# Kernel tuning notes

Measured on AMD Instinct MI355X. Metric: run time of the kernel, lower is better.

## Reference

```python
import jax, jax.numpy as jnp
import numpy as np

B, C, H, W = 32, 256, 8, 8
N = H * W                      # n_objects = 64
D_G_IN = 2 * C + 2             # pair concat + 2-dim relative position = 514
HG = 512                       # g hidden / output dim
HF = 512                       # f hidden dim
D_OUT = 256                    # f output dim


def _relative_grid_feat():
    # feat[p, q, 0] = oh(p) - oh(q); feat[p, q, 1] = ow(p) - ow(q); zero-centered globally
    idx = jnp.arange(N)
    oh, ow = idx // W, idx % W
    r0 = (oh[:, None] - oh[None, :]).astype(jnp.float32)
    r1 = (ow[:, None] - ow[None, :]).astype(jnp.float32)
    rel = jnp.stack([r0, r1], axis=-1)  # [N, N, 2]
    return rel - rel.mean()


def setup_inputs() -> dict:
    key = jax.random.key(0)
    ks = jax.random.split(key, 11)
    s = 0.02
    return {
        "x": jax.random.normal(ks[0], (B, C, H, W), dtype=jnp.float32),
        "g_W0": jax.random.normal(ks[1], (D_G_IN, HG), dtype=jnp.float32) * s,
        "g_b0": jnp.zeros((HG,), dtype=jnp.float32),
        "g_W1": jax.random.normal(ks[2], (HG, HG), dtype=jnp.float32) * s,
        "g_b1": jnp.zeros((HG,), dtype=jnp.float32),
        "g_W2": jax.random.normal(ks[3], (HG, HG), dtype=jnp.float32) * s,
        "g_b2": jnp.zeros((HG,), dtype=jnp.float32),
        "f_W0": jax.random.normal(ks[4], (HG, HF), dtype=jnp.float32) * s,
        "f_b0": jnp.zeros((HF,), dtype=jnp.float32),
        "f_W1": jax.random.normal(ks[5], (HF, D_OUT), dtype=jnp.float32) * s,
        "f_b1": jnp.zeros((D_OUT,), dtype=jnp.float32),
    }


def reference(x, g_W0, g_b0, g_W1, g_b1, g_W2, g_b2, f_W0, f_b0, f_W1, f_b1):
    relu = jax.nn.relu
    x_flat = x.reshape(B, C, N)                     # [B, C, N]
    xT = jnp.transpose(x_flat, (0, 2, 1))           # [B, N, C]
    # pair index k = p*N + q: xi takes object q (inner), xj takes object p (outer)
    xi = jnp.broadcast_to(xT[:, None, :, :], (B, N, N, C))
    xj = jnp.broadcast_to(xT[:, :, None, :], (B, N, N, C))
    rel = jnp.broadcast_to(_relative_grid_feat()[None], (B, N, N, 2))
    pair = jnp.concatenate([xi, xj, rel], axis=-1)  # [B, N, N, 2C+2]
    # g MLP (nonlinear=True -> activation on output too)
    h = relu(jnp.einsum('bpqd,dh->bpqh', pair, g_W0) + g_b0)
    h = relu(jnp.einsum('bpqh,hk->bpqk', h, g_W1) + g_b1)
    relations = relu(jnp.einsum('bpqh,hk->bpqk', h, g_W2) + g_b2)  # [B, N, N, HG]
    embedding = relations.sum(axis=(1, 2))          # sum over all pairs -> [B, HG]
    # f MLP (linear output)
    hf = relu(embedding @ f_W0 + f_b0)
    out = hf @ f_W1 + f_b1                          # [B, D_OUT]
    return out
```

## Files before the change

kernel.cpp:

```cpp
#include <hip/hip_runtime.h>


typedef short short8 __attribute__((ext_vector_type(8)));
typedef float f32x16 __attribute__((ext_vector_type(16)));

__device__ __forceinline__ unsigned short f2bf(float f) {
    unsigned u = __builtin_bit_cast(unsigned, f);
    u = (u + 0x7FFFu + ((u >> 16) & 1u)) >> 16;
    return (unsigned short)u;
}

__device__ __forceinline__ unsigned cvt_pk(float a, float b) {
    unsigned r;
    asm("v_cvt_pk_bf16_f32 %0, %1, %2" : "=v"(r) : "v"(a), "v"(b));
    return r;
}

__global__ __launch_bounds__(512) void uv_kernel(
    const float* __restrict__ x, const float* __restrict__ W0,
    const float* __restrict__ b0, float* __restrict__ Up, float* __restrict__ Vp)
{
    __shared__ float xs[256 * 8];
    const int blk = blockIdx.x;
    const int b = blk >> 3, n0 = (blk & 7) * 8;
    const int tid = threadIdx.x;

    for (int i = tid; i < 2048; i += 512) {
        int c = i >> 3, r = i & 7;
        xs[i] = x[((size_t)b * 256 + c) * 64 + n0 + r];
    }
    __syncthreads();

    const int h = tid;
    float ua[8], va[8];
#pragma unroll
    for (int r = 0; r < 8; ++r) { ua[r] = 0.f; va[r] = 0.f; }

    for (int c = 0; c < 256; ++c) {
        float wa = W0[(size_t)c * 512 + h];
        float wb = W0[(size_t)(256 + c) * 512 + h];
#pragma unroll
        for (int r = 0; r < 8; ++r) {
            float xv = xs[c * 8 + r];
            ua[r] += xv * wa;
            va[r] += xv * wb;
        }
    }
    const float w2a = W0[(size_t)512 * 512 + h];
    const float w2b = W0[(size_t)513 * 512 + h];
    const float bb = b0[h];
#pragma unroll
    for (int r = 0; r < 8; ++r) {
        int n = n0 + r;
        float fh = (float)(n >> 3), fw = (float)(n & 7);
        Up[((size_t)b * 64 + n) * 512 + h] = ua[r] - fh * w2a - fw * w2b;
        Vp[((size_t)b * 64 + n) * 512 + h] = va[r] + fh * w2a + fw * w2b + bb;
    }
}

__global__ __launch_bounds__(256) void wswz_kernel(
    const float* __restrict__ W1, const float* __restrict__ W2,
    unsigned short* __restrict__ W1s, unsigned short* __restrict__ W2s,
    float* __restrict__ emb)
{
    int gid = blockIdx.x * 256 + threadIdx.x;
    if (gid < 16384) emb[gid] = 0.f;
    int m = gid >> 15;
    int idx = gid & 32767;
    int col = idx & 511;
    int kg = idx >> 9;
    const float* W = m ? W2 : W1;
    unsigned short* O = m ? W2s : W1s;
    short8 v;
#pragma unroll
    for (int j = 0; j < 8; ++j)
        v[j] = (short)f2bf(W[(size_t)(kg * 8 + j) * 512 + col]);
    *(short8*)(O + (size_t)idx * 8) = v;
}

__global__ __launch_bounds__(512, 2) void main_kernel(
    const float* __restrict__ Up, const float* __restrict__ Vp,
    const unsigned short* __restrict__ W1s, const unsigned short* __restrict__ W2s,
    const float* __restrict__ b1, const float* __restrict__ b2,
    float* __restrict__ emb)
{
    extern __shared__ __align__(16) unsigned char lds[];
    unsigned char* T[2] = { lds, lds + 65536 };

    const int wg = ((blockIdx.x & 7) << 7) | (blockIdx.x >> 3);
    const int b = wg >> 5, pp = wg & 31;
    const int p0 = pp * 2, p1 = p0 + 1;

    const int tid = threadIdx.x;
    const int lane = tid & 63, wave = tid >> 6;
    const int l31 = lane & 31, lg = lane >> 5;
    const int swz = (l31 & 15) << 4;
    const int wcol = wave * 64;

    {
        const int cc = tid & 63;
        const int r0 = tid >> 6;
        const float* vA = Vp + ((size_t)(b * 64 + p0)) * 512 + cc * 8;
        const float* vB = Vp + ((size_t)(b * 64 + p1)) * 512 + cc * 8;
        float4 vA0 = *(const float4*)(vA),     vA1 = *(const float4*)(vA + 4);
        float4 vB0 = *(const float4*)(vB),     vB1 = *(const float4*)(vB + 4);
#pragma unroll
        for (int it = 0; it < 8; ++it) {
            int row = r0 + it * 8;
            const float* ub = Up + ((size_t)(b * 64 + row)) * 512 + cc * 8;
            float4 u0 = *(const float4*)(ub);
            float4 u1 = *(const float4*)(ub + 4);
            int off = row * 1024 + ((cc * 16) ^ ((row & 15) << 4));
            uint4 w;
            w.x = cvt_pk(fmaxf(u0.x + vA0.x, 0.f), fmaxf(u0.y + vA0.y, 0.f));
            w.y = cvt_pk(fmaxf(u0.z + vA0.z, 0.f), fmaxf(u0.w + vA0.w, 0.f));
            w.z = cvt_pk(fmaxf(u1.x + vA1.x, 0.f), fmaxf(u1.y + vA1.y, 0.f));
            w.w = cvt_pk(fmaxf(u1.z + vA1.z, 0.f), fmaxf(u1.w + vA1.w, 0.f));
            *(uint4*)(&T[0][off]) = w;
            w.x = cvt_pk(fmaxf(u0.x + vB0.x, 0.f), fmaxf(u0.y + vB0.y, 0.f));
            w.y = cvt_pk(fmaxf(u0.z + vB0.z, 0.f), fmaxf(u0.w + vB0.w, 0.f));
            w.z = cvt_pk(fmaxf(u1.x + vB1.x, 0.f), fmaxf(u1.y + vB1.y, 0.f));
            w.w = cvt_pk(fmaxf(u1.z + vB1.z, 0.f), fmaxf(u1.w + vB1.w, 0.f));
            *(uint4*)(&T[1][off]) = w;
        }
    }
    __syncthreads();

    const int arow0 = l31 * 1024;
    const int arow1 = (l31 + 32) * 1024;

    f32x16 acc[2][2][2];
#pragma unroll
    for (int t = 0; t < 2; ++t)
#pragma unroll
        for (int i = 0; i < 2; ++i)
#pragma unroll
            for (int j = 0; j < 2; ++j) acc[t][i][j] = (f32x16)0.f;

    __builtin_amdgcn_s_setprio(1);
#pragma unroll 2
    for (int ks = 0; ks < 32; ++ks) {
        int achunk = (ks * 32 + lg * 16) ^ swz;
        short8 a00 = *(const short8*)(&T[0][arow0 + achunk]);
        short8 a01 = *(const short8*)(&T[0][arow1 + achunk]);
        short8 a10 = *(const short8*)(&T[1][arow0 + achunk]);
        short8 a11 = *(const short8*)(&T[1][arow1 + achunk]);
        const unsigned short* bp = W1s + ((size_t)((ks * 2 + lg) * 512 + wcol + l31)) * 8;
        short8 wv0 = *(const short8*)(bp);
        short8 wv1 = *(const short8*)(bp + 32 * 8);
        acc[0][0][0] = __builtin_amdgcn_mfma_f32_32x32x16_bf16(wv0, a00, acc[0][0][0], 0, 0, 0);
        acc[0][1][0] = __builtin_amdgcn_mfma_f32_32x32x16_bf16(wv1, a00, acc[0][1][0], 0, 0, 0);
        acc[0][0][1] = __builtin_amdgcn_mfma_f32_32x32x16_bf16(wv0, a01, acc[0][0][1], 0, 0, 0);
        acc[0][1][1] = __builtin_amdgcn_mfma_f32_32x32x16_bf16(wv1, a01, acc[0][1][1], 0, 0, 0);
        acc[1][0][0] = __builtin_amdgcn_mfma_f32_32x32x16_bf16(wv0, a10, acc[1][0][0], 0, 0, 0);
        acc[1][1][0] = __builtin_amdgcn_mfma_f32_32x32x16_bf16(wv1, a10, acc[1][1][0], 0, 0, 0);
        acc[1][0][1] = __builtin_amdgcn_mfma_f32_32x32x16_bf16(wv0, a11, acc[1][0][1], 0, 0, 0);
        acc[1][1][1] = __builtin_amdgcn_mfma_f32_32x32x16_bf16(wv1, a11, acc[1][1][1], 0, 0, 0);
    }
    __builtin_amdgcn_s_setprio(0);
    __syncthreads();

    {
#pragma unroll
        for (int hf = 0; hf < 2; ++hf) {
#pragma unroll
            for (int g = 0; g < 4; ++g) {
                int h = wcol + hf * 32 + g * 8 + 4 * lg;
                float4 bb = *(const float4*)(b1 + h);
#pragma unroll
                for (int t = 0; t < 2; ++t) {
#pragma unroll
                    for (int qf = 0; qf < 2; ++qf) {
                        int q = qf * 32 + l31;
                        float a0 = fmaxf(acc[t][hf][qf][g * 4 + 0] + bb.x, 0.f);
                        float a1 = fmaxf(acc[t][hf][qf][g * 4 + 1] + bb.y, 0.f);
                        float a2 = fmaxf(acc[t][hf][qf][g * 4 + 2] + bb.z, 0.f);
                        float a3 = fmaxf(acc[t][hf][qf][g * 4 + 3] + bb.w, 0.f);
                        uint2 pk;
                        pk.x = cvt_pk(a0, a1);
                        pk.y = cvt_pk(a2, a3);
                        int off = q * 1024 + ((h * 2) ^ ((q & 15) << 4));
                        *(uint2*)(&T[t][off]) = pk;
                    }
                }
            }
        }
    }
    __syncthreads();

    f32x16 acc2[2][2][2];
#pragma unroll
    for (int t = 0; t < 2; ++t)
#pragma unroll
        for (int i = 0; i < 2; ++i)
#pragma unroll
            for (int j = 0; j < 2; ++j) acc2[t][i][j] = (f32x16)0.f;

    __builtin_amdgcn_s_setprio(1);
#pragma unroll 2
    for (int ks = 0; ks < 32; ++ks) {
        int achunk = (ks * 32 + lg * 16) ^ swz;
        short8 a00 = *(const short8*)(&T[0][arow0 + achunk]);
        short8 a01 = *(const short8*)(&T[0][arow1 + achunk]);
        short8 a10 = *(const short8*)(&T[1][arow0 + achunk]);
        short8 a11 = *(const short8*)(&T[1][arow1 + achunk]);
        const unsigned short* bp = W2s + ((size_t)((ks * 2 + lg) * 512 + wcol + l31)) * 8;
        short8 bv0 = *(const short8*)(bp);
        short8 bv1 = *(const short8*)(bp + 32 * 8);
        acc2[0][0][0] = __builtin_amdgcn_mfma_f32_32x32x16_bf16(a00, bv0, acc2[0][0][0], 0, 0, 0);
        acc2[0][1][0] = __builtin_amdgcn_mfma_f32_32x32x16_bf16(a01, bv0, acc2[0][1][0], 0, 0, 0);
        acc2[0][0][1] = __builtin_amdgcn_mfma_f32_32x32x16_bf16(a00, bv1, acc2[0][0][1], 0, 0, 0);
        acc2[0][1][1] = __builtin_amdgcn_mfma_f32_32x32x16_bf16(a01, bv1, acc2[0][1][1], 0, 0, 0);
        acc2[1][0][0] = __builtin_amdgcn_mfma_f32_32x32x16_bf16(a10, bv0, acc2[1][0][0], 0, 0, 0);
        acc2[1][1][0] = __builtin_amdgcn_mfma_f32_32x32x16_bf16(a11, bv0, acc2[1][1][0], 0, 0, 0);
        acc2[1][0][1] = __builtin_amdgcn_mfma_f32_32x32x16_bf16(a10, bv1, acc2[1][0][1], 0, 0, 0);
        acc2[1][1][1] = __builtin_amdgcn_mfma_f32_32x32x16_bf16(a11, bv1, acc2[1][1][1], 0, 0, 0);
    }
    __builtin_amdgcn_s_setprio(0);

    {
        float s[2];
#pragma unroll
        for (int cf = 0; cf < 2; ++cf) {
            int col = wcol + cf * 32 + l31;
            float bias = b2[col];
            float tt = 0.f;
#pragma unroll
            for (int t = 0; t < 2; ++t)
#pragma unroll
                for (int rf = 0; rf < 2; ++rf)
#pragma unroll
                    for (int reg = 0; reg < 16; ++reg)
                        tt += fmaxf(acc2[t][rf][cf][reg] + bias, 0.f);
            tt += __shfl_xor(tt, 32);
            s[cf] = tt;
        }
        if (lane < 32) {
            unsafeAtomicAdd(&emb[b * 512 + wcol + lane], s[0]);
            unsafeAtomicAdd(&emb[b * 512 + wcol + 32 + lane], s[1]);
        }
    }
}

__global__ __launch_bounds__(256) void f0_kernel(
    const float* __restrict__ emb, const float* __restrict__ fW0,
    const float* __restrict__ fb0, float* __restrict__ hs)
{
    __shared__ float es[512];
    __shared__ float red[256];
    const int b = blockIdx.x >> 3, s = blockIdx.x & 7;
    const int t = threadIdx.x;
    const int colL = t & 63, cg = t >> 6;
    es[t] = emb[b * 512 + t];
    es[t + 256] = emb[b * 512 + 256 + t];
    __syncthreads();
    const int col = s * 64 + colL;
    float a = 0.f;
    const int c0 = cg * 128;
#pragma unroll 4
    for (int c = c0; c < c0 + 128; ++c)
        a += es[c] * fW0[(size_t)c * 512 + col];
    red[t] = a;
    __syncthreads();
    if (t < 64) {
        float r = red[t] + red[t + 64] + red[t + 128] + red[t + 192] + fb0[col];
        hs[b * 512 + col] = fmaxf(r, 0.f);
    }
}

__global__ __launch_bounds__(256) void f1_kernel(
    const float* __restrict__ hs, const float* __restrict__ fW1,
    const float* __restrict__ fb1, float* __restrict__ out)
{
    __shared__ float es[512];
    __shared__ float red[256];
    const int b = blockIdx.x >> 2, s = blockIdx.x & 3;
    const int t = threadIdx.x;
    const int colL = t & 63, cg = t >> 6;
    es[t] = hs[b * 512 + t];
    es[t + 256] = hs[b * 512 + 256 + t];
    __syncthreads();
    const int col = s * 64 + colL;
    float a = 0.f;
    const int c0 = cg * 128;
#pragma unroll 4
    for (int c = c0; c < c0 + 128; ++c)
        a += es[c] * fW1[(size_t)c * 256 + col];
    red[t] = a;
    __syncthreads();
    if (t < 64) {
        out[b * 256 + col] = red[t] + red[t + 64] + red[t + 128] + red[t + 192] + fb1[col];
    }
}

extern "C" void kernel_launch(void* const* d_in, const int* in_sizes, int n_in,
                              void* d_out, int out_size, void* d_ws, size_t ws_size,
                              hipStream_t stream)
{
    const float* x   = (const float*)d_in[0];
    const float* gW0 = (const float*)d_in[1];
    const float* gb0 = (const float*)d_in[2];
    const float* gW1 = (const float*)d_in[3];
    const float* gb1 = (const float*)d_in[4];
    const float* gW2 = (const float*)d_in[5];
    const float* gb2 = (const float*)d_in[6];
    const float* fW0 = (const float*)d_in[7];
    const float* fb0 = (const float*)d_in[8];
    const float* fW1 = (const float*)d_in[9];
    const float* fb1 = (const float*)d_in[10];
    float* out = (float*)d_out;

    char* ws = (char*)d_ws;
    float* Up           = (float*)(ws);
    float* Vp           = (float*)(ws + (4 << 20));
    unsigned short* W1s = (unsigned short*)(ws + (8 << 20));
    unsigned short* W2s = (unsigned short*)(ws + (8 << 20) + (512 << 10));
    float* emb          = (float*)(ws + (9 << 20));
    float* hs           = (float*)(ws + (9 << 20) + (64 << 10));

    uv_kernel<<<256, 512, 0, stream>>>(x, gW0, gb0, Up, Vp);
    wswz_kernel<<<256, 256, 0, stream>>>(gW1, gW2, W1s, W2s, emb);
    main_kernel<<<1024, 512, 131072, stream>>>(Up, Vp, W1s, W2s, gb1, gb2, emb);
    f0_kernel<<<256, 256, 0, stream>>>(emb, fW0, fb0, hs);
    f1_kernel<<<128, 256, 0, stream>>>(hs, fW1, fb1, out);
}
```

Before: 177.8 us.

## Split main kernel work across 16 waves, one pair-tile per wave group

The main kernel grows from 512 to 1024 threads per block. Each wave now handles a single p-tile (t = wave&1) instead of both, which halves the accumulator registers per wave and doubles the waves available to hide latency. Weight fragments are software-prefetched one k-step ahead in a fully unrolled loop, and the U-row loads in the prologue are batched. The uv_kernel channel loop also gets an unroll-4 pragma. The trade-off is that weight loads from global memory are now duplicated across the two waves that share a column block, and the 1024-thread blocks must still fit in the register budget.

```diff
diff --git a/kernel.cpp b/kernel.cpp
--- a/kernel.cpp
+++ b/kernel.cpp
@@ -36,6 +36,7 @@
 #pragma unroll
     for (int r = 0; r < 8; ++r) { ua[r] = 0.f; va[r] = 0.f; }
 
+#pragma unroll 4
     for (int c = 0; c < 256; ++c) {
         float wa = W0[(size_t)c * 512 + h];
         float wb = W0[(size_t)(256 + c) * 512 + h];
@@ -78,50 +79,50 @@
     *(short8*)(O + (size_t)idx * 8) = v;
 }
 
-__global__ __launch_bounds__(512, 2) void main_kernel(
+__global__ __launch_bounds__(1024, 4) void main_kernel(
     const float* __restrict__ Up, const float* __restrict__ Vp,
     const unsigned short* __restrict__ W1s, const unsigned short* __restrict__ W2s,
     const float* __restrict__ b1, const float* __restrict__ b2,
     float* __restrict__ emb)
 {
     extern __shared__ __align__(16) unsigned char lds[];
-    unsigned char* T[2] = { lds, lds + 65536 };
 
     const int wg = ((blockIdx.x & 7) << 7) | (blockIdx.x >> 3);
     const int b = wg >> 5, pp = wg & 31;
-    const int p0 = pp * 2, p1 = p0 + 1;
 
     const int tid = threadIdx.x;
     const int lane = tid & 63, wave = tid >> 6;
     const int l31 = lane & 31, lg = lane >> 5;
     const int swz = (l31 & 15) << 4;
-    const int wcol = wave * 64;
-
-    {
+    const int t = wave & 1;
+    const int wcol = (wave >> 1) << 6;
+    unsigned char* T = lds + t * 65536;
+
+    {
+        const int bt = tid >> 9;
         const int cc = tid & 63;
-        const int r0 = tid >> 6;
-        const float* vA = Vp + ((size_t)(b * 64 + p0)) * 512 + cc * 8;
-        const float* vB = Vp + ((size_t)(b * 64 + p1)) * 512 + cc * 8;
-        float4 vA0 = *(const float4*)(vA),     vA1 = *(const float4*)(vA + 4);
-        float4 vB0 = *(const float4*)(vB),     vB1 = *(const float4*)(vB + 4);
+        const int r0 = (tid >> 6) & 7;
+        const int p = pp * 2 + bt;
+        unsigned char* TB = lds + bt * 65536;
+        float4 u0[8], u1[8];
+#pragma unroll
+        for (int it = 0; it < 8; ++it) {
+            const float* ub = Up + ((size_t)(b * 64 + r0 + it * 8)) * 512 + cc * 8;
+            u0[it] = *(const float4*)(ub);
+            u1[it] = *(const float4*)(ub + 4);
+        }
+        const float* vp = Vp + ((size_t)(b * 64 + p)) * 512 + cc * 8;
+        float4 v0 = *(const float4*)(vp), v1 = *(const float4*)(vp + 4);
 #pragma unroll
         for (int it = 0; it < 8; ++it) {
             int row = r0 + it * 8;
-            const float* ub = Up + ((size_t)(b * 64 + row)) * 512 + cc * 8;
-            float4 u0 = *(const float4*)(ub);
-            float4 u1 = *(const float4*)(ub + 4);
             int off = row * 1024 + ((cc * 16) ^ ((row & 15) << 4));
             uint4 w;
-            w.x = cvt_pk(fmaxf(u0.x + vA0.x, 0.f), fmaxf(u0.y + vA0.y, 0.f));
-            w.y = cvt_pk(fmaxf(u0.z + vA0.z, 0.f), fmaxf(u0.w + vA0.w, 0.f));
-            w.z = cvt_pk(fmaxf(u1.x + vA1.x, 0.f), fmaxf(u1.y + vA1.y, 0.f));
-            w.w = cvt_pk(fmaxf(u1.z + vA1.z, 0.f), fmaxf(u1.w + vA1.w, 0.f));
-            *(uint4*)(&T[0][off]) = w;
-            w.x = cvt_pk(fmaxf(u0.x + vB0.x, 0.f), fmaxf(u0.y + vB0.y, 0.f));
-            w.y = cvt_pk(fmaxf(u0.z + vB0.z, 0.f), fmaxf(u0.w + vB0.w, 0.f));
-            w.z = cvt_pk(fmaxf(u1.x + vB1.x, 0.f), fmaxf(u1.y + vB1.y, 0.f));
-            w.w = cvt_pk(fmaxf(u1.z + vB1.z, 0.f), fmaxf(u1.w + vB1.w, 0.f));
-            *(uint4*)(&T[1][off]) = w;
+            w.x = cvt_pk(fmaxf(u0[it].x + v0.x, 0.f), fmaxf(u0[it].y + v0.y, 0.f));
+            w.y = cvt_pk(fmaxf(u0[it].z + v0.z, 0.f), fmaxf(u0[it].w + v0.w, 0.f));
+            w.z = cvt_pk(fmaxf(u1[it].x + v1.x, 0.f), fmaxf(u1[it].y + v1.y, 0.f));
+            w.w = cvt_pk(fmaxf(u1[it].z + v1.z, 0.f), fmaxf(u1[it].w + v1.w, 0.f));
+            *(uint4*)(&TB[off]) = w;
         }
     }
     __syncthreads();
@@ -129,35 +130,35 @@
     const int arow0 = l31 * 1024;
     const int arow1 = (l31 + 32) * 1024;
 
-    f32x16 acc[2][2][2];
-#pragma unroll
-    for (int t = 0; t < 2; ++t)
-#pragma unroll
-        for (int i = 0; i < 2; ++i)
-#pragma unroll
-            for (int j = 0; j < 2; ++j) acc[t][i][j] = (f32x16)0.f;
-
-    __builtin_amdgcn_s_setprio(1);
-#pragma unroll 2
-    for (int ks = 0; ks < 32; ++ks) {
-        int achunk = (ks * 32 + lg * 16) ^ swz;
-        short8 a00 = *(const short8*)(&T[0][arow0 + achunk]);
-        short8 a01 = *(const short8*)(&T[0][arow1 + achunk]);
-        short8 a10 = *(const short8*)(&T[1][arow0 + achunk]);
-        short8 a11 = *(const short8*)(&T[1][arow1 + achunk]);
-        const unsigned short* bp = W1s + ((size_t)((ks * 2 + lg) * 512 + wcol + l31)) * 8;
-        short8 wv0 = *(const short8*)(bp);
-        short8 wv1 = *(const short8*)(bp + 32 * 8);
-        acc[0][0][0] = __builtin_amdgcn_mfma_f32_32x32x16_bf16(wv0, a00, acc[0][0][0], 0, 0, 0);
-        acc[0][1][0] = __builtin_amdgcn_mfma_f32_32x32x16_bf16(wv1, a00, acc[0][1][0], 0, 0, 0);
-        acc[0][0][1] = __builtin_amdgcn_mfma_f32_32x32x16_bf16(wv0, a01, acc[0][0][1], 0, 0, 0);
-        acc[0][1][1] = __builtin_amdgcn_mfma_f32_32x32x16_bf16(wv1, a01, acc[0][1][1], 0, 0, 0);
-        acc[1][0][0] = __builtin_amdgcn_mfma_f32_32x32x16_bf16(wv0, a10, acc[1][0][0], 0, 0, 0);
-        acc[1][1][0] = __builtin_amdgcn_mfma_f32_32x32x16_bf16(wv1, a10, acc[1][1][0], 0, 0, 0);
-        acc[1][0][1] = __builtin_amdgcn_mfma_f32_32x32x16_bf16(wv0, a11, acc[1][0][1], 0, 0, 0);
-        acc[1][1][1] = __builtin_amdgcn_mfma_f32_32x32x16_bf16(wv1, a11, acc[1][1][1], 0, 0, 0);
-    }
-    __builtin_amdgcn_s_setprio(0);
+    f32x16 acc[2][2];
+#pragma unroll
+    for (int i = 0; i < 2; ++i)
+#pragma unroll
+        for (int j = 0; j < 2; ++j) acc[i][j] = (f32x16)0.f;
+
+    {
+        const unsigned short* wb = W1s + ((size_t)(lg * 512 + wcol + l31)) * 8;
+        short8 wn0 = *(const short8*)(wb);
+        short8 wn1 = *(const short8*)(wb + 256);
+        __builtin_amdgcn_s_setprio(1);
+#pragma unroll
+        for (int ks = 0; ks < 32; ++ks) {
+            short8 cw0 = wn0, cw1 = wn1;
+            if (ks < 31) {
+                const unsigned short* np = wb + (size_t)(ks + 1) * 8192;
+                wn0 = *(const short8*)(np);
+                wn1 = *(const short8*)(np + 256);
+            }
+            int achunk = (ks * 32 + lg * 16) ^ swz;
+            short8 a0 = *(const short8*)(&T[arow0 + achunk]);
+            short8 a1 = *(const short8*)(&T[arow1 + achunk]);
+            acc[0][0] = __builtin_amdgcn_mfma_f32_32x32x16_bf16(cw0, a0, acc[0][0], 0, 0, 0);
+            acc[1][0] = __builtin_amdgcn_mfma_f32_32x32x16_bf16(cw1, a0, acc[1][0], 0, 0, 0);
+            acc[0][1] = __builtin_amdgcn_mfma_f32_32x32x16_bf16(cw0, a1, acc[0][1], 0, 0, 0);
+            acc[1][1] = __builtin_amdgcn_mfma_f32_32x32x16_bf16(cw1, a1, acc[1][1], 0, 0, 0);
+        }
+        __builtin_amdgcn_s_setprio(0);
+    }
     __syncthreads();
 
     {
@@ -168,55 +169,52 @@
                 int h = wcol + hf * 32 + g * 8 + 4 * lg;
                 float4 bb = *(const float4*)(b1 + h);
 #pragma unroll
-                for (int t = 0; t < 2; ++t) {
-#pragma unroll
-                    for (int qf = 0; qf < 2; ++qf) {
-                        int q = qf * 32 + l31;
-                        float a0 = fmaxf(acc[t][hf][qf][g * 4 + 0] + bb.x, 0.f);
-                        float a1 = fmaxf(acc[t][hf][qf][g * 4 + 1] + bb.y, 0.f);
-                        float a2 = fmaxf(acc[t][hf][qf][g * 4 + 2] + bb.z, 0.f);
-                        float a3 = fmaxf(acc[t][hf][qf][g * 4 + 3] + bb.w, 0.f);
-                        uint2 pk;
-                        pk.x = cvt_pk(a0, a1);
-                        pk.y = cvt_pk(a2, a3);
-                        int off = q * 1024 + ((h * 2) ^ ((q & 15) << 4));
-                        *(uint2*)(&T[t][off]) = pk;
-                    }
+                for (int qf = 0; qf < 2; ++qf) {
+                    int q = qf * 32 + l31;
+                    float a0 = fmaxf(acc[hf][qf][g * 4 + 0] + bb.x, 0.f);
+                    float a1 = fmaxf(acc[hf][qf][g * 4 + 1] + bb.y, 0.f);
+                    float a2 = fmaxf(acc[hf][qf][g * 4 + 2] + bb.z, 0.f);
+                    float a3 = fmaxf(acc[hf][qf][g * 4 + 3] + bb.w, 0.f);
+                    uint2 pk;
+                    pk.x = cvt_pk(a0, a1);
+                    pk.y = cvt_pk(a2, a3);
+                    int off = q * 1024 + ((h * 2) ^ ((q & 15) << 4));
+                    *(uint2*)(&T[off]) = pk;
                 }
             }
         }
     }
     __syncthreads();
 
-    f32x16 acc2[2][2][2];
-#pragma unroll
-    for (int t = 0; t < 2; ++t)
-#pragma unroll
-        for (int i = 0; i < 2; ++i)
-#pragma unroll
-            for (int j = 0; j < 2; ++j) acc2[t][i][j] = (f32x16)0.f;
-
-    __builtin_amdgcn_s_setprio(1);
-#pragma unroll 2
-    for (int ks = 0; ks < 32; ++ks) {
-        int achunk = (ks * 32 + lg * 16) ^ swz;
-        short8 a00 = *(const short8*)(&T[0][arow0 + achunk]);
-        short8 a01 = *(const short8*)(&T[0][arow1 + achunk]);
-        short8 a10 = *(const short8*)(&T[1][arow0 + achunk]);
-        short8 a11 = *(const short8*)(&T[1][arow1 + achunk]);
-        const unsigned short* bp = W2s + ((size_t)((ks * 2 + lg) * 512 + wcol + l31)) * 8;
-        short8 bv0 = *(const short8*)(bp);
-        short8 bv1 = *(const short8*)(bp + 32 * 8);
-        acc2[0][0][0] = __builtin_amdgcn_mfma_f32_32x32x16_bf16(a00, bv0, acc2[0][0][0], 0, 0, 0);
-        acc2[0][1][0] = __builtin_amdgcn_mfma_f32_32x32x16_bf16(a01, bv0, acc2[0][1][0], 0, 0, 0);
-        acc2[0][0][1] = __builtin_amdgcn_mfma_f32_32x32x16_bf16(a00, bv1, acc2[0][0][1], 0, 0, 0);
-        acc2[0][1][1] = __builtin_amdgcn_mfma_f32_32x32x16_bf16(a01, bv1, acc2[0][1][1], 0, 0, 0);
-        acc2[1][0][0] = __builtin_amdgcn_mfma_f32_32x32x16_bf16(a10, bv0, acc2[1][0][0], 0, 0, 0);
-        acc2[1][1][0] = __builtin_amdgcn_mfma_f32_32x32x16_bf16(a11, bv0, acc2[1][1][0], 0, 0, 0);
-        acc2[1][0][1] = __builtin_amdgcn_mfma_f32_32x32x16_bf16(a10, bv1, acc2[1][0][1], 0, 0, 0);
-        acc2[1][1][1] = __builtin_amdgcn_mfma_f32_32x32x16_bf16(a11, bv1, acc2[1][1][1], 0, 0, 0);
-    }
-    __builtin_amdgcn_s_setprio(0);
+    f32x16 acc2[2][2];
+#pragma unroll
+    for (int i = 0; i < 2; ++i)
+#pragma unroll
+        for (int j = 0; j < 2; ++j) acc2[i][j] = (f32x16)0.f;
+
+    {
+        const unsigned short* wb = W2s + ((size_t)(lg * 512 + wcol + l31)) * 8;
+        short8 wn0 = *(const short8*)(wb);
+        short8 wn1 = *(const short8*)(wb + 256);
+        __builtin_amdgcn_s_setprio(1);
+#pragma unroll
+        for (int ks = 0; ks < 32; ++ks) {
+            short8 cw0 = wn0, cw1 = wn1;
+            if (ks < 31) {
+                const unsigned short* np = wb + (size_t)(ks + 1) * 8192;
+                wn0 = *(const short8*)(np);
+                wn1 = *(const short8*)(np + 256);
+            }
+            int achunk = (ks * 32 + lg * 16) ^ swz;
+            short8 a0 = *(const short8*)(&T[arow0 + achunk]);
+            short8 a1 = *(const short8*)(&T[arow1 + achunk]);
+            acc2[0][0] = __builtin_amdgcn_mfma_f32_32x32x16_bf16(a0, cw0, acc2[0][0], 0, 0, 0);
+            acc2[1][0] = __builtin_amdgcn_mfma_f32_32x32x16_bf16(a1, cw0, acc2[1][0], 0, 0, 0);
+            acc2[0][1] = __builtin_amdgcn_mfma_f32_32x32x16_bf16(a0, cw1, acc2[0][1], 0, 0, 0);
+            acc2[1][1] = __builtin_amdgcn_mfma_f32_32x32x16_bf16(a1, cw1, acc2[1][1], 0, 0, 0);
+        }
+        __builtin_amdgcn_s_setprio(0);
+    }
 
     {
         float s[2];
@@ -226,12 +224,10 @@
             float bias = b2[col];
             float tt = 0.f;
 #pragma unroll
-            for (int t = 0; t < 2; ++t)
-#pragma unroll
-                for (int rf = 0; rf < 2; ++rf)
-#pragma unroll
-                    for (int reg = 0; reg < 16; ++reg)
-                        tt += fmaxf(acc2[t][rf][cf][reg] + bias, 0.f);
+            for (int qf = 0; qf < 2; ++qf)
+#pragma unroll
+                for (int reg = 0; reg < 16; ++reg)
+                    tt += fmaxf(acc2[qf][cf][reg] + bias, 0.f);
             tt += __shfl_xor(tt, 32);
             s[cf] = tt;
         }
@@ -320,7 +316,7 @@
 
     uv_kernel<<<256, 512, 0, stream>>>(x, gW0, gb0, Up, Vp);
     wswz_kernel<<<256, 256, 0, stream>>>(gW1, gW2, W1s, W2s, emb);
-    main_kernel<<<1024, 512, 131072, stream>>>(Up, Vp, W1s, W2s, gb1, gb2, emb);
+    main_kernel<<<1024, 1024, 131072, stream>>>(Up, Vp, W1s, W2s, gb1, gb2, emb);
     f0_kernel<<<256, 256, 0, stream>>>(emb, fW0, fb0, hs);
     f1_kernel<<<128, 256, 0, stream>>>(hs, fW1, fb1, out);
 }
```

Result: slower. 185.5 us (+4.4%).
